# Kernel tuning notes

Measured on AMD Instinct MI355X. Metric: run time of the kernel, lower is better.

## Reference

```python
import jax, jax.numpy as jnp
import numpy as np

N_NODES, N_EDGES, N_ROOTS = 32768, 131072, 1024
VOCAB, EMB_D, FEAT = 50000, 256, 128
SEQ, HEADS, OUT_CH = 16, 16, 125
KERNELS = (5, 6, 7, 8)


def _add_self_loops(edge_index, n):
    loop = jnp.arange(n, dtype=edge_index.dtype)
    src = jnp.concatenate([edge_index[0], loop])
    dst = jnp.concatenate([edge_index[1], loop])
    return src, dst


def _gat_conv(x, W, a_src, a_dst, b, src, dst, n):
    # PyG GATConv (heads=1): h=xW, e_ij = LeakyReLU(a_s.h_j + a_d.h_i), softmax over incoming edges of i
    h = x @ W                                   # [N, F]
    al_s = h @ a_src                            # [N]
    al_d = h @ a_dst                            # [N]
    e = jax.nn.leaky_relu(al_s[src] + al_d[dst], 0.2)   # [E+N]
    m = jax.ops.segment_max(e, dst, num_segments=n)
    ex = jnp.exp(e - m[dst])
    den = jax.ops.segment_sum(ex, dst, num_segments=n)
    coef = ex / den[dst]
    out = jax.ops.segment_sum(coef[:, None] * h[src], dst, num_segments=n)
    return out + b


def _gcn_conv(x, W, b, src, dst, n):
    h = x @ W
    ones = jnp.ones_like(src, dtype=x.dtype)
    deg = jax.ops.segment_sum(ones, dst, num_segments=n)
    dinv = jax.lax.rsqrt(jnp.maximum(deg, 1.0))
    norm = dinv[src] * dinv[dst]                # [E+N]
    out = jax.ops.segment_sum(norm[:, None] * h[src], dst, num_segments=n)
    return out + b


def _transformer_block(x, Wq, bq, Wk, bk, Wv, bv, Wo, bo, g, be):
    # multi-head self-attention + output proj + residual + layernorm (attn_dropout=0)
    n, s, d = x.shape
    dh = d // HEADS
    q = (x @ Wq + bq).reshape(n, s, HEADS, dh)
    k = (x @ Wk + bk).reshape(n, s, HEADS, dh)
    v = (x @ Wv + bv).reshape(n, s, HEADS, dh)
    att = jnp.einsum('nqhd,nkhd->nhqk', q, k) / np.sqrt(dh).astype(np.float32)
    att = jax.nn.softmax(att, axis=-1)
    o = jnp.einsum('nhqk,nkhd->nqhd', att, v).reshape(n, s, d)
    o = o @ Wo + bo
    y = x + o
    mu = jnp.mean(y, axis=-1, keepdims=True)
    var = jnp.var(y, axis=-1, keepdims=True)
    return (y - mu) * jax.lax.rsqrt(var + 1e-5) * g + be


def _conv_branch(t, ws, bs):
    # t: [N, D, S]; Conv1d VALID + ReLU + max-pool over full output length
    feats = []
    for w, b in zip(ws, bs):
        a = jax.lax.conv_general_dilated(t, w, (1,), 'VALID',
                                         dimension_numbers=('NCH', 'OIH', 'NCH'))
        a = jax.nn.relu(a + b[:, None])
        feats.append(jnp.max(a, axis=-1))       # [N, OUT_CH]
    return jnp.concatenate(feats, axis=1)        # [N, 4*OUT_CH]


def _forward(x2, emb, Wq, bq, Wk, bk, Wv, bv, Wo, bo, ln_g, ln_b,
             gat1_W, gat1_as, gat1_ad, gat1_b, gcn1_W, gcn1_b,
             gat2_W, gat2_as, gat2_ad, gat2_b, gcn2_W, gcn2_b,
             conv_w0, conv_b0, conv_w1, conv_b1, conv_w2, conv_b2, conv_w3, conv_b3,
             fc1_W, fc1_b, fc2_W, fc2_b,
             text2, edge_index, root_index, rootpost_index):
    n = x2.shape[0]
    src, dst = _add_self_loops(edge_index, n)

    stance_graph = _gat_conv(x2, gat1_W, gat1_as, gat1_ad, gat1_b, src, dst, n)
    stance_shared = _gcn_conv(x2, gcn1_W, gcn1_b, src, dst, n)

    t = emb[text2]                                            # [N, S, D]
    t = _transformer_block(t, Wq, bq, Wk, bk, Wv, bv, Wo, bo, ln_g, ln_b)
    t_avg = jnp.mean(t, axis=1)                               # [N, D]

    cat = jnp.concatenate([stance_graph, stance_shared, t_avg], axis=1)  # [N, 2F+D]
    stance_graph2 = _gat_conv(cat, gat2_W, gat2_as, gat2_ad, gat2_b, src, dst, n)
    _ = _gcn_conv(stance_shared, gcn2_W, gcn2_b, src, dst, n)  # computed but unused in forward (faithful)

    tc = jnp.transpose(t, (0, 2, 1))                          # [N, D, S]
    text_feat = _conv_branch(tc, (conv_w0, conv_w1, conv_w2, conv_w3),
                             (conv_b0, conv_b1, conv_b2, conv_b3))  # [N, 500]

    final = jnp.concatenate([stance_graph2[root_index],
                             text_feat[root_index],
                             text_feat[rootpost_index]], axis=1)     # [B, F+1000]
    h = jax.nn.relu(final @ fc1_W + fc1_b)
    return h @ fc2_W + fc2_b                                  # [B, 3]


def setup_inputs() -> dict:
    key = jax.random.key(0)
    ks = iter(jax.random.split(key, 48))
    s = 0.05
    inp = {}
    inp['x2'] = jax.random.normal(next(ks), (N_NODES, FEAT), jnp.float32)
    inp['emb'] = jax.random.normal(next(ks), (VOCAB, EMB_D), jnp.float32) * s
    for nm in ['Wq', 'Wk', 'Wv', 'Wo']:
        inp[nm] = jax.random.normal(next(ks), (EMB_D, EMB_D), jnp.float32) * s
    for nm in ['bq', 'bk', 'bv', 'bo']:
        inp[nm] = jnp.zeros((EMB_D,), jnp.float32)
    inp['ln_g'] = jnp.ones((EMB_D,), jnp.float32)
    inp['ln_b'] = jnp.zeros((EMB_D,), jnp.float32)
    inp['gat1_W'] = jax.random.normal(next(ks), (FEAT, FEAT), jnp.float32) * s
    inp['gat1_as'] = jax.random.normal(next(ks), (FEAT,), jnp.float32) * s
    inp['gat1_ad'] = jax.random.normal(next(ks), (FEAT,), jnp.float32) * s
    inp['gat1_b'] = jnp.zeros((FEAT,), jnp.float32)
    inp['gcn1_W'] = jax.random.normal(next(ks), (FEAT, FEAT), jnp.float32) * s
    inp['gcn1_b'] = jnp.zeros((FEAT,), jnp.float32)
    inp['gat2_W'] = jax.random.normal(next(ks), (2 * FEAT + EMB_D, FEAT), jnp.float32) * s
    inp['gat2_as'] = jax.random.normal(next(ks), (FEAT,), jnp.float32) * s
    inp['gat2_ad'] = jax.random.normal(next(ks), (FEAT,), jnp.float32) * s
    inp['gat2_b'] = jnp.zeros((FEAT,), jnp.float32)
    inp['gcn2_W'] = jax.random.normal(next(ks), (FEAT, FEAT), jnp.float32) * s
    inp['gcn2_b'] = jnp.zeros((FEAT,), jnp.float32)
    for i, K in enumerate(KERNELS):
        inp[f'conv_w{i}'] = jax.random.normal(next(ks), (OUT_CH, EMB_D, K), jnp.float32) * s
        inp[f'conv_b{i}'] = jnp.zeros((OUT_CH,), jnp.float32)
    inp['fc1_W'] = jax.random.normal(next(ks), (FEAT + 8 * OUT_CH, 300), jnp.float32) * s
    inp['fc1_b'] = jnp.zeros((300,), jnp.float32)
    inp['fc2_W'] = jax.random.normal(next(ks), (300, 3), jnp.float32) * s
    inp['fc2_b'] = jnp.zeros((3,), jnp.float32)
    inp['text2'] = jax.random.randint(next(ks), (N_NODES, SEQ), 0, VOCAB, jnp.int32)
    inp['edge_index'] = jax.random.randint(next(ks), (2, N_EDGES), 0, N_NODES, jnp.int32)
    inp['root_index'] = jax.random.randint(next(ks), (N_ROOTS,), 0, N_NODES, jnp.int32)
    inp['rootpost_index'] = jax.random.randint(next(ks), (N_ROOTS,), 0, N_NODES, jnp.int32)
    return inp


def reference(x2, emb, Wq, bq, Wk, bk, Wv, bv, Wo, bo, ln_g, ln_b,
              gat1_W, gat1_as, gat1_ad, gat1_b, gcn1_W, gcn1_b,
              gat2_W, gat2_as, gat2_ad, gat2_b, gcn2_W, gcn2_b,
              conv_w0, conv_b0, conv_w1, conv_b1, conv_w2, conv_b2, conv_w3, conv_b3,
              fc1_W, fc1_b, fc2_W, fc2_b,
              text2, edge_index, root_index, rootpost_index):
    return _forward(x2, emb, Wq, bq, Wk, bk, Wv, bv, Wo, bo, ln_g, ln_b,
                    gat1_W, gat1_as, gat1_ad, gat1_b, gcn1_W, gcn1_b,
                    gat2_W, gat2_as, gat2_ad, gat2_b, gcn2_W, gcn2_b,
                    conv_w0, conv_b0, conv_w1, conv_b1, conv_w2, conv_b2, conv_w3, conv_b3,
                    fc1_W, fc1_b, fc2_W, fc2_b,
                    text2, edge_index, root_index, rootpost_index)
```

## Files before the change

### kernel.cpp

```cpp
#include <hip/hip_runtime.h>
#include <hip/hip_bf16.h>
#include <cstdint>
#include <cstddef>

#define N_NODES 32768
#define N_EDGES 131072
#define ET_EDGES (N_EDGES + N_NODES)
#define N_ROOTS 1024
#define EMB_D 256
#define FEAT 128
#define SEQ 16
#define OUT_CH 125

static inline int cdiv(long long a, long long b) { return (int)((a + b - 1) / b); }

typedef short short8 __attribute__((ext_vector_type(8)));
typedef short short4v __attribute__((ext_vector_type(4)));
typedef float f32x4 __attribute__((ext_vector_type(4)));

__device__ __forceinline__ float warpReduceSum(float v) {
#pragma unroll
    for (int m = 32; m; m >>= 1) v += __shfl_xor(v, m, 64);
    return v;
}
__device__ __forceinline__ int encf(float f) {
    int i = __float_as_int(f);
    return i >= 0 ? i : (i ^ 0x7fffffff);
}
__device__ __forceinline__ float decf(int i) {
    return __int_as_float(i >= 0 ? i : (i ^ 0x7fffffff));
}
__device__ __forceinline__ short f2bs(float x) {
    unsigned u = __float_as_uint(x);
    u += 0x7fffu + ((u >> 16) & 1u);
    return (short)(u >> 16);
}
__device__ __forceinline__ short2 f2bs2(float a, float b) {
    union {
        __hip_bfloat162 h;
        short2 s;
    } u;
    u.h = __float22bfloat162_rn(make_float2(a, b));
    return u.s;
}
__device__ __forceinline__ float bs2f(short s) {
    return __uint_as_float(((unsigned)(unsigned short)s) << 16);
}

__global__ void fill_i32(int* p, int v, int n) {
    int i = blockIdx.x * 256 + threadIdx.x;
    if (i < n) p[i] = v;
}

__global__ void init_cat(float* __restrict__ cat, const float* __restrict__ b1, const float* __restrict__ b2) {
    int i = blockIdx.x * 256 + threadIdx.x;
    int n = i >> 8, c = i & 255;
    float b = (c < 128) ? b1[c] : b2[c - 128];
    cat[(size_t)n * 512 + c] = b;
}

__global__ void repack_wall(const float* __restrict__ cw0, const float* __restrict__ cw1,
                            const float* __restrict__ cw2, const float* __restrict__ cw3,
                            __hip_bfloat16* __restrict__ wall) {
    int i = blockIdx.x * 256 + threadIdx.x;
    if (i >= 512 * 2048) return;
    int r = i >> 11, c = i & 2047;
    int k = c >> 8, ic = c & 255;
    float v = 0.f;
    if (r < 500) {
        int Kidx = r / 125, oc = r - Kidx * 125;
        int K = 5 + Kidx;
        if (k < K) {
            const float* cw = Kidx == 0 ? cw0 : Kidx == 1 ? cw1 : Kidx == 2 ? cw2 : cw3;
            v = cw[((size_t)oc * 256 + ic) * K + k];
        }
    }
    wall[i] = __float2bfloat16(v);
}

__global__ void repack_xf(const float* __restrict__ Wq, const float* __restrict__ Wk, const float* __restrict__ Wv,
                          const float* __restrict__ Wo, const float* __restrict__ bq, const float* __restrict__ bk,
                          const float* __restrict__ bv, short* __restrict__ wqkvT, short* __restrict__ woT,
                          float* __restrict__ bqkv) {
    int i = blockIdx.x * 256 + threadIdx.x;
    if (i < 768 * 256) {
        int n = i >> 8, k = i & 255;
        const float* W = n < 256 ? Wq : n < 512 ? Wk : Wv;
        wqkvT[i] = f2bs(W[k * 256 + (n & 255)]);
    }
    if (i < 256 * 256) {
        int n = i >> 8, k = i & 255;
        woT[i] = f2bs(Wo[k * 256 + n]);
    }
    if (i < 768) bqkv[i] = i < 256 ? bq[i] : i < 512 ? bk[i - 256] : bv[i - 512];
}

__global__ __launch_bounds__(256) void gemm64(const float* __restrict__ A, const float* __restrict__ B,
                                              const float* __restrict__ bias, float* __restrict__ C,
                                              int M, int N, int K, int lda, int ldc, int doRelu) {
    __shared__ float As[16][65];
    __shared__ float Bs[16][65];
    const int bm = blockIdx.y * 64, bn = blockIdx.x * 64;
    const int tid = threadIdx.x;
    const int tx = tid & 15, ty = tid >> 4;
    float acc[4][4] = {};
    for (int k0 = 0; k0 < K; k0 += 16) {
#pragma unroll
        for (int j = 0; j < 4; j++) {
            int i = tid + j * 256;
            int kk = i & 15, m = i >> 4;
            int gr = bm + m, gc = k0 + kk;
            As[kk][m] = (gr < M && gc < K) ? A[(size_t)gr * lda + gc] : 0.f;
        }
#pragma unroll
        for (int j = 0; j < 4; j++) {
            int i = tid + j * 256;
            int n = i & 63, kk = i >> 6;
            int gr = k0 + kk, gc = bn + n;
            Bs[kk][n] = (gr < K && gc < N) ? B[(size_t)gr * N + gc] : 0.f;
        }
        __syncthreads();
#pragma unroll
        for (int kk = 0; kk < 16; kk++) {
            float a[4], b[4];
#pragma unroll
            for (int i2 = 0; i2 < 4; i2++) a[i2] = As[kk][ty * 4 + i2];
#pragma unroll
            for (int j2 = 0; j2 < 4; j2++) b[j2] = Bs[kk][tx * 4 + j2];
#pragma unroll
            for (int i2 = 0; i2 < 4; i2++)
#pragma unroll
                for (int j2 = 0; j2 < 4; j2++) acc[i2][j2] = fmaf(a[i2], b[j2], acc[i2][j2]);
        }
        __syncthreads();
    }
#pragma unroll
    for (int i2 = 0; i2 < 4; i2++) {
        int r = bm + ty * 4 + i2;
        if (r >= M) continue;
#pragma unroll
        for (int j2 = 0; j2 < 4; j2++) {
            int c = bn + tx * 4 + j2;
            if (c >= N) continue;
            float v = acc[i2][j2];
            if (bias) v += bias[c];
            if (doRelu) v = fmaxf(v, 0.f);
            C[(size_t)r * ldc + c] = v;
        }
    }
}

__global__ __launch_bounds__(256) void alpha_kernel(const float* __restrict__ h, const float* __restrict__ asrc,
                                                    const float* __restrict__ adst, float* __restrict__ als,
                                                    float* __restrict__ ald) {
    int gw = (blockIdx.x * 256 + threadIdx.x) >> 6;
    int lane = threadIdx.x & 63;
    if (gw >= N_NODES) return;
    const float* row = h + (size_t)gw * FEAT;
    float v0 = row[lane], v1 = row[lane + 64];
    float ps = v0 * asrc[lane] + v1 * asrc[lane + 64];
    float pd = v0 * adst[lane] + v1 * adst[lane + 64];
    ps = warpReduceSum(ps);
    pd = warpReduceSum(pd);
    if (lane == 0) {
        als[gw] = ps;
        ald[gw] = pd;
    }
}

__device__ __forceinline__ void edge_decode(int i, const int* __restrict__ ei, int& s, int& d) {
    if (i < N_EDGES) {
        s = ei[i];
        d = ei[N_EDGES + i];
    } else {
        s = d = i - N_EDGES;
    }
}

__global__ void edge_p1(const int* __restrict__ ei, const float* __restrict__ als, const float* __restrict__ ald,
                        float* __restrict__ elog, int* __restrict__ menc, float* dega) {
    int i = blockIdx.x * 256 + threadIdx.x;
    if (i >= ET_EDGES) return;
    int s, d;
    edge_decode(i, ei, s, d);
    float e = als[s] + ald[d];
    e = (e >= 0.f) ? e : 0.2f * e;
    elog[i] = e;
    atomicMax(&menc[d], encf(e));
    if (dega) unsafeAtomicAdd(&dega[d], 1.f);
}

__global__ void edge_p2(const int* __restrict__ ei, float* __restrict__ elog, const int* __restrict__ menc,
                        float* __restrict__ den) {
    int i = blockIdx.x * 256 + threadIdx.x;
    if (i >= ET_EDGES) return;
    int s, d;
    edge_decode(i, ei, s, d);
    float ex = __expf(elog[i] - decf(menc[d]));
    elog[i] = ex;
    unsafeAtomicAdd(&den[d], ex);
}

__global__ void edge_p2b(const int* __restrict__ ei, float* __restrict__ elog, const float* __restrict__ den) {
    int i = blockIdx.x * 256 + threadIdx.x;
    if (i >= ET_EDGES) return;
    int s, d;
    edge_decode(i, ei, s, d);
    elog[i] = elog[i] / den[d];
}

__global__ void dinv_kernel(float* deg) {
    int i = blockIdx.x * 256 + threadIdx.x;
    if (i < N_NODES) deg[i] = rsqrtf(fmaxf(deg[i], 1.f));
}

__global__ void edge_scatter(const int* __restrict__ ei, const float* __restrict__ coef, const float* __restrict__ h,
                             float* __restrict__ out, int ldo) {
    int i = blockIdx.x * 256 + threadIdx.x;
    if (i >= ET_EDGES * FEAT) return;
    int e = i >> 7, f = i & 127;
    int s, d;
    edge_decode(e, ei, s, d);
    unsafeAtomicAdd(&out[(size_t)d * ldo + f], coef[e] * h[(size_t)s * FEAT + f]);
}

__global__ void gcn_scatter(const int* __restrict__ ei, const float* __restrict__ dinv, const float* __restrict__ h,
                            float* __restrict__ out, int ldo) {
    int i = blockIdx.x * 256 + threadIdx.x;
    if (i >= ET_EDGES * FEAT) return;
    int e = i >> 7, f = i & 127;
    int s, d;
    edge_decode(e, ei, s, d);
    float coef = dinv[s] * dinv[d];
    unsafeAtomicAdd(&out[(size_t)d * ldo + f], coef * h[(size_t)s * FEAT + f]);
}

__global__ void root_gather(const float* __restrict__ g2, const int* __restrict__ rooti, const float* __restrict__ gb,
                            float* __restrict__ fin) {
    int i = blockIdx.x * 256 + threadIdx.x;
    if (i >= N_ROOTS * FEAT) return;
    int r = i >> 7, c = i & 127;
    fin[(size_t)r * 1128 + c] = g2[(size_t)rooti[r] * FEAT + c] + gb[c];
}

__global__ void fc2_kernel(const float* __restrict__ fch, const float* __restrict__ W, const float* __restrict__ b,
                           float* __restrict__ out) {
    int i = blockIdx.x * 256 + threadIdx.x;
    if (i >= N_ROOTS * 3) return;
    int r = i / 3, c = i - r * 3;
    float acc = b[c];
    for (int k = 0; k < 300; k++) acc = fmaf(fch[(size_t)r * 300 + k], W[k * 3 + c], acc);
    out[i] = acc;
}

#define QA_STRIDE 264
#define KR_STRIDE 264

template <int MODE>
__global__ __launch_bounds__(256, 4) void xformer_kernel(
    const float* __restrict__ emb, const int* __restrict__ text2, const short* __restrict__ wqkvT,
    const float* __restrict__ bqkv, const short* __restrict__ woT, const float* __restrict__ bo,
    const float* __restrict__ lng, const float* __restrict__ lnb, const int* __restrict__ rooti,
    const int* __restrict__ rpi, float* __restrict__ cat, unsigned short* __restrict__ tbuf) {
    __shared__ short qa[32 * QA_STRIDE];
    __shared__ short kreg[32 * KR_STRIDE];

    const int tid = threadIdx.x;
    const int wave = tid >> 6, lane = tid & 63;
    const int quad = lane >> 4, l16 = lane & 15;

    int gnode[2];
#pragma unroll
    for (int m = 0; m < 2; m++) {
        int slot = blockIdx.x * 2 + m;
        gnode[m] = (MODE == 0) ? slot : ((slot < N_ROOTS) ? rooti[slot] : rpi[slot - N_ROOTS]);
    }
    const int tokA0 = text2[gnode[0] * SEQ + l16];
    const int tokA1 = text2[gnode[1] * SEQ + l16];

    short8 Areg[2][8];
#pragma unroll
    for (int k0 = 0; k0 < 8; k0++) {
        const float* pa0 = emb + (size_t)tokA0 * 256 + k0 * 32 + quad * 8;
        const float* pa1 = emb + (size_t)tokA1 * 256 + k0 * 32 + quad * 8;
        float4 a0l = ((const float4*)pa0)[0], a0h = ((const float4*)pa0)[1];
        float4 a1l = ((const float4*)pa1)[0], a1h = ((const float4*)pa1)[1];
        short2 c0 = f2bs2(a0l.x, a0l.y), c1 = f2bs2(a0l.z, a0l.w), c2 = f2bs2(a0h.x, a0h.y), c3 = f2bs2(a0h.z, a0h.w);
        Areg[0][k0] = (short8){c0.x, c0.y, c1.x, c1.y, c2.x, c2.y, c3.x, c3.y};
        c0 = f2bs2(a1l.x, a1l.y);
        c1 = f2bs2(a1l.z, a1l.w);
        c2 = f2bs2(a1h.x, a1h.y);
        c3 = f2bs2(a1h.z, a1h.w);
        Areg[1][k0] = (short8){c0.x, c0.y, c1.x, c1.y, c2.x, c2.y, c3.x, c3.y};
    }

    f32x4 vacc[4][2];

#pragma unroll
    for (int grp = 0; grp < 3; grp++) {
        f32x4 acc[4][2];
#pragma unroll
        for (int i = 0; i < 4; i++) {
            acc[i][0] = (f32x4){0.f, 0.f, 0.f, 0.f};
            acc[i][1] = (f32x4){0.f, 0.f, 0.f, 0.f};
        }
#pragma unroll
        for (int k0 = 0; k0 < 8; k0++) {
#pragma unroll
            for (int i = 0; i < 4; i++) {
                const int g = grp * 16 + wave * 4 + i;
                short8 B = *(const short8*)(wqkvT + (size_t)(g * 16 + l16) * 256 + k0 * 32 + quad * 8);
                acc[i][0] = __builtin_amdgcn_mfma_f32_16x16x32_bf16(Areg[0][k0], B, acc[i][0], 0, 0, 0);
                acc[i][1] = __builtin_amdgcn_mfma_f32_16x16x32_bf16(Areg[1][k0], B, acc[i][1], 0, 0, 0);
            }
        }
#pragma unroll
        for (int i = 0; i < 4; i++) {
            const int g = grp * 16 + wave * 4 + i;
            const int col = g * 16 + l16;
            const float b = bqkv[col];
            if (grp == 2) {
#pragma unroll
                for (int m = 0; m < 2; m++) {
                    vacc[i][m][0] = acc[i][m][0] + b;
                    vacc[i][m][1] = acc[i][m][1] + b;
                    vacc[i][m][2] = acc[i][m][2] + b;
                    vacc[i][m][3] = acc[i][m][3] + b;
                }
            } else {
#pragma unroll
                for (int m = 0; m < 2; m++) {
                    const int rbase = m * 16 + quad * 4;
                    float v0 = acc[i][m][0] + b, v1 = acc[i][m][1] + b;
                    float v2 = acc[i][m][2] + b, v3 = acc[i][m][3] + b;
                    if (grp == 0) {
                        v0 *= 0.25f;
                        v1 *= 0.25f;
                        v2 *= 0.25f;
                        v3 *= 0.25f;
                    }
                    short2 p01 = f2bs2(v0, v1), p23 = f2bs2(v2, v3);
                    short* dst = (grp == 0) ? (qa + (rbase)*QA_STRIDE + col) : (kreg + (rbase)*KR_STRIDE + (col - 256));
                    const int str = (grp == 0) ? QA_STRIDE : KR_STRIDE;
                    dst[0 * str] = p01.x;
                    dst[1 * str] = p01.y;
                    dst[2 * str] = p23.x;
                    dst[3 * str] = p23.y;
                }
            }
        }
    }

#pragma unroll
    for (int p = 0; p < 2; p++) {
#pragma unroll
        for (int i = 0; i < 4; i++) {
            const int h = wave * 4 + i;
            const int arow = p * 16 + l16;
            const int q8 = (quad & 1) * 8;
            short8 Af = *(const short8*)(kreg + arow * KR_STRIDE + h * 16 + q8);
            short8 Bf = *(const short8*)(qa + arow * QA_STRIDE + h * 16 + q8);
            if (quad >= 2) {
                Af = (short8){0, 0, 0, 0, 0, 0, 0, 0};
                Bf = (short8){0, 0, 0, 0, 0, 0, 0, 0};
            }
            f32x4 S = __builtin_amdgcn_mfma_f32_16x16x32_bf16(Af, Bf, (f32x4){0.f, 0.f, 0.f, 0.f}, 0, 0, 0);
            float mx = fmaxf(fmaxf(S[0], S[1]), fmaxf(S[2], S[3]));
            mx = fmaxf(mx, __shfl_xor(mx, 16));
            mx = fmaxf(mx, __shfl_xor(mx, 32));
            float e0 = __expf(S[0] - mx), e1 = __expf(S[1] - mx);
            float e2 = __expf(S[2] - mx), e3 = __expf(S[3] - mx);
            float sm = (e0 + e1) + (e2 + e3);
            sm += __shfl_xor(sm, 16);
            sm += __shfl_xor(sm, 32);
            const float inv = 1.f / sm;
            float pr[4] = {e0 * inv, e1 * inv, e2 * inv, e3 * inv};
            float bp[8];
#pragma unroll
            for (int j = 0; j < 8; j++) {
                const int srcq = (2 * quad + (j >> 2)) & 3;
                float v = __shfl(pr[j & 3], l16 + 16 * srcq);
                bp[j] = (quad < 2) ? v : 0.f;
            }
            short2 b01 = f2bs2(bp[0], bp[1]), b23 = f2bs2(bp[2], bp[3]);
            short2 b45 = f2bs2(bp[4], bp[5]), b67 = f2bs2(bp[6], bp[7]);
            short8 BP = (short8){b01.x, b01.y, b23.x, b23.y, b45.x, b45.y, b67.x, b67.y};
            float av[8];
#pragma unroll
            for (int j = 0; j < 8; j++) {
                const int srcq = ((quad & 1) * 2 + (j >> 2));
                float v = __shfl(vacc[i][p][j & 3], l16 + 16 * srcq);
                av[j] = (quad < 2) ? v : 0.f;
            }
            short2 a01 = f2bs2(av[0], av[1]), a23 = f2bs2(av[2], av[3]);
            short2 a45 = f2bs2(av[4], av[5]), a67 = f2bs2(av[6], av[7]);
            short8 Av = (short8){a01.x, a01.y, a23.x, a23.y, a45.x, a45.y, a67.x, a67.y};
            f32x4 O = __builtin_amdgcn_mfma_f32_16x16x32_bf16(Av, BP, (f32x4){0.f, 0.f, 0.f, 0.f}, 0, 0, 0);
            short2 o01 = f2bs2(O[0], O[1]), o23 = f2bs2(O[2], O[3]);
            *(short4v*)(qa + arow * QA_STRIDE + h * 16 + quad * 4) = (short4v){o01.x, o01.y, o23.x, o23.y};
        }
    }
    __syncthreads();

    {
        short8 Afr[2][8];
#pragma unroll
        for (int m = 0; m < 2; m++)
#pragma unroll
            for (int k0 = 0; k0 < 8; k0++)
                Afr[m][k0] = *(const short8*)(qa + (m * 16 + l16) * QA_STRIDE + k0 * 32 + quad * 8);
#pragma unroll
        for (int i = 0; i < 4; i++) {
            const int g = wave * 4 + i;
            f32x4 oa0 = (f32x4){0.f, 0.f, 0.f, 0.f}, oa1 = (f32x4){0.f, 0.f, 0.f, 0.f};
#pragma unroll
            for (int k0 = 0; k0 < 8; k0++) {
                short8 B = *(const short8*)(woT + (size_t)(g * 16 + l16) * 256 + k0 * 32 + quad * 8);
                oa0 = __builtin_amdgcn_mfma_f32_16x16x32_bf16(Afr[0][k0], B, oa0, 0, 0, 0);
                oa1 = __builtin_amdgcn_mfma_f32_16x16x32_bf16(Afr[1][k0], B, oa1, 0, 0, 0);
            }
            const int col = g * 16 + l16;
            const float bocol = bo[col];
            short2 a01 = f2bs2(oa0[0] + bocol, oa0[1] + bocol), a23 = f2bs2(oa0[2] + bocol, oa0[3] + bocol);
            short2 c01 = f2bs2(oa1[0] + bocol, oa1[1] + bocol), c23 = f2bs2(oa1[2] + bocol, oa1[3] + bocol);
            kreg[(quad * 4 + 0) * KR_STRIDE + col] = a01.x;
            kreg[(quad * 4 + 1) * KR_STRIDE + col] = a01.y;
            kreg[(quad * 4 + 2) * KR_STRIDE + col] = a23.x;
            kreg[(quad * 4 + 3) * KR_STRIDE + col] = a23.y;
            kreg[(16 + quad * 4 + 0) * KR_STRIDE + col] = c01.x;
            kreg[(16 + quad * 4 + 1) * KR_STRIDE + col] = c01.y;
            kreg[(16 + quad * 4 + 2) * KR_STRIDE + col] = c23.x;
            kreg[(16 + quad * 4 + 3) * KR_STRIDE + col] = c23.y;
        }
    }
    __syncthreads();

    float* qs = (float*)qa;
    {
        const int row = tid >> 3, seg = tid & 7;
        const int m = row >> 4, r = row & 15;
        const int tokr = text2[gnode[m] * SEQ + r];
        const float* ep = emb + (size_t)tokr * 256 + seg * 32;
        float sum = 0.f, sq = 0.f;
#pragma unroll
        for (int j = 0; j < 4; j++) {
            short8 y8 = *(const short8*)(kreg + row * KR_STRIDE + seg * 32 + j * 8);
            float4 ea = ((const float4*)(ep + j * 8))[0];
            float4 eb = ((const float4*)(ep + j * 8))[1];
            float ev[8] = {ea.x, ea.y, ea.z, ea.w, eb.x, eb.y, eb.z, eb.w};
            float yv[8];
#pragma unroll
            for (int e = 0; e < 8; e++) {
                yv[e] = bs2f(y8[e]) + ev[e];
                sum += yv[e];
                sq = fmaf(yv[e], yv[e], sq);
            }
            short2 w0 = f2bs2(yv[0], yv[1]), w1 = f2bs2(yv[2], yv[3]);
            short2 w2 = f2bs2(yv[4], yv[5]), w3 = f2bs2(yv[6], yv[7]);
            *(short4v*)(kreg + row * KR_STRIDE + seg * 32 + j * 8) = (short4v){w0.x, w0.y, w1.x, w1.y};
            *(short4v*)(kreg + row * KR_STRIDE + seg * 32 + j * 8 + 4) = (short4v){w2.x, w2.y, w3.x, w3.y};
        }
        qs[tid] = sum;
        qs[256 + tid] = sq;
    }
    __syncthreads();
    if (tid < 32) {
        float s = 0.f, q2 = 0.f;
#pragma unroll
        for (int j = 0; j < 8; j++) {
            s += qs[tid * 8 + j];
            q2 += qs[256 + tid * 8 + j];
        }
        float mu = s * (1.f / 256.f);
        float var = q2 * (1.f / 256.f) - mu * mu;
        qs[512 + tid * 2] = mu;
        qs[512 + tid * 2 + 1] = rsqrtf(var + 1e-5f);
    }
    __syncthreads();
    {
        const int c = tid;
        const float g = lng[c], bb = lnb[c];
        float csum[2] = {0.f, 0.f};
#pragma unroll
        for (int m = 0; m < 2; m++) {
#pragma unroll
            for (int r = 0; r < 16; r++) {
                const int row = m * 16 + r;
                const float yv = bs2f(kreg[row * KR_STRIDE + c]);
                const float mu = qs[512 + row * 2], rstd = qs[512 + row * 2 + 1];
                const float o = (yv - mu) * rstd * g + bb;
                if (MODE == 0) {
                    csum[m] += o;
                } else {
                    tbuf[((size_t)(blockIdx.x * 2 + m) * 24 + r) * 256 + c] = (unsigned short)f2bs(o);
                }
            }
        }
        if (MODE == 0) {
            cat[(size_t)gnode[0] * 512 + 256 + c] = csum[0] * (1.f / 16.f);
            cat[(size_t)gnode[1] * 512 + 256 + c] = csum[1] * (1.f / 16.f);
        } else {
            for (int z = tid; z < 2 * 8 * 256; z += 256) {
                const int m = z >> 11, rem = z & 2047;
                tbuf[((size_t)(blockIdx.x * 2 + m) * 24 + 16 + (rem >> 8)) * 256 + (rem & 255)] = 0;
            }
        }
    }
}

__global__ __launch_bounds__(256) void conv_gemm(const short* __restrict__ tb, const short* __restrict__ wall,
                                                 float* __restrict__ C) {
    __shared__ short As[128 * 40];
    __shared__ short Bs[128 * 40];
    const int bid = blockIdx.x;
    const int m0 = (bid >> 2) * 128;
    const int n0 = (bid & 3) * 128;
    const int tid = threadIdx.x;
    const int lane = tid & 63;
    const int wave = tid >> 6;
    const int wm = (wave >> 1) * 64, wn = (wave & 1) * 64;
    const int quad = lane >> 4, l16 = lane & 15;

    const int r0 = tid >> 2, kc = (tid & 3) * 8;
    const int r1 = r0 + 64;
    const int am0 = m0 + r0, am1 = m0 + r1;
    const int s0 = am0 / 12, p0_ = am0 - s0 * 12;
    const int s1 = am1 / 12, p1_ = am1 - s1 * 12;
    const size_t ga0 = (size_t)(s0 * 24 + p0_) * 256 + kc;
    const size_t ga1 = (size_t)(s1 * 24 + p1_) * 256 + kc;
    const size_t gb0 = (size_t)(n0 + r0) * 2048 + kc;
    const size_t gb1 = (size_t)(n0 + r1) * 2048 + kc;
    short* sa0 = As + r0 * 40 + kc;
    short* sa1 = As + r1 * 40 + kc;
    short* sb0 = Bs + r0 * 40 + kc;
    short* sb1 = Bs + r1 * 40 + kc;

    f32x4 acc[4][4];
#pragma unroll
    for (int i = 0; i < 4; i++)
#pragma unroll
        for (int j = 0; j < 4; j++) acc[i][j] = (f32x4){0.f, 0.f, 0.f, 0.f};

    for (int k0 = 0; k0 < 2048; k0 += 32) {
        short8 a0 = *(const short8*)(tb + ga0 + k0);
        short8 a1 = *(const short8*)(tb + ga1 + k0);
        short8 b0 = *(const short8*)(wall + gb0 + k0);
        short8 b1 = *(const short8*)(wall + gb1 + k0);
        *(short8*)sa0 = a0;
        *(short8*)sa1 = a1;
        *(short8*)sb0 = b0;
        *(short8*)sb1 = b1;
        __syncthreads();
        short8 af[4], bfr[4];
#pragma unroll
        for (int i = 0; i < 4; i++) af[i] = *(const short8*)(As + (wm + i * 16 + l16) * 40 + quad * 8);
#pragma unroll
        for (int j = 0; j < 4; j++) bfr[j] = *(const short8*)(Bs + (wn + j * 16 + l16) * 40 + quad * 8);
#pragma unroll
        for (int i = 0; i < 4; i++)
#pragma unroll
            for (int j = 0; j < 4; j++)
                acc[i][j] = __builtin_amdgcn_mfma_f32_16x16x32_bf16(af[i], bfr[j], acc[i][j], 0, 0, 0);
        __syncthreads();
    }
#pragma unroll
    for (int i = 0; i < 4; i++) {
#pragma unroll
        for (int j = 0; j < 4; j++) {
            const int col = n0 + wn + j * 16 + l16;
            const size_t base = (size_t)(m0 + wm + i * 16 + quad * 4) * 512 + col;
#pragma unroll
            for (int r = 0; r < 4; r++) C[base + (size_t)r * 512] = acc[i][j][r];
        }
    }
}

__global__ void conv_maxpool(const float* __restrict__ C, const float* __restrict__ cb0, const float* __restrict__ cb1,
                             const float* __restrict__ cb2, const float* __restrict__ cb3, float* __restrict__ fin) {
    int i = blockIdx.x * 256 + threadIdx.x;
    if (i >= 2048 * 500) return;
    int slot = i / 500, q = i - slot * 500;
    int Kidx = q / 125, oc = q - Kidx * 125;
    int L = 12 - Kidx;
    const float* base = C + (size_t)(slot * 12) * 512 + q;
    float m = base[0];
    for (int p = 1; p < L; p++) m = fmaxf(m, base[(size_t)p * 512]);
    float b = (Kidx == 0 ? cb0 : Kidx == 1 ? cb1 : Kidx == 2 ? cb2 : cb3)[oc];
    float v = fmaxf(m + b, 0.f);
    int idx = slot < N_ROOTS ? slot : slot - N_ROOTS;
    int colbase = slot < N_ROOTS ? 128 : 628;
    fin[(size_t)idx * 1128 + colbase + q] = v;
}

extern "C" void kernel_launch(void* const* d_in, const int* in_sizes, int n_in, void* d_out, int out_size, void* d_ws,
                              size_t ws_size, hipStream_t stream) {
    const float* x2 = (const float*)d_in[0];
    const float* emb = (const float*)d_in[1];
    const float* Wq = (const float*)d_in[2];
    const float* Wk = (const float*)d_in[3];
    const float* Wv = (const float*)d_in[4];
    const float* Wo = (const float*)d_in[5];
    const float* bq = (const float*)d_in[6];
    const float* bk = (const float*)d_in[7];
    const float* bv = (const float*)d_in[8];
    const float* bo = (const float*)d_in[9];
    const float* lng = (const float*)d_in[10];
    const float* lnb = (const float*)d_in[11];
    const float* gat1_W = (const float*)d_in[12];
    const float* gat1_as = (const float*)d_in[13];
    const float* gat1_ad = (const float*)d_in[14];
    const float* gat1_b = (const float*)d_in[15];
    const float* gcn1_W = (const float*)d_in[16];
    const float* gcn1_b = (const float*)d_in[17];
    const float* gat2_W = (const float*)d_in[18];
    const float* gat2_as = (const float*)d_in[19];
    const float* gat2_ad = (const float*)d_in[20];
    const float* gat2_b = (const float*)d_in[21];
    const float* cw0 = (const float*)d_in[24];
    const float* cb0 = (const float*)d_in[25];
    const float* cw1 = (const float*)d_in[26];
    const float* cb1 = (const float*)d_in[27];
    const float* cw2 = (const float*)d_in[28];
    const float* cb2 = (const float*)d_in[29];
    const float* cw3 = (const float*)d_in[30];
    const float* cb3 = (const float*)d_in[31];
    const float* fc1_W = (const float*)d_in[32];
    const float* fc1_b = (const float*)d_in[33];
    const float* fc2_W = (const float*)d_in[34];
    const float* fc2_b = (const float*)d_in[35];
    const int* text2 = (const int*)d_in[36];
    const int* ei = (const int*)d_in[37];
    const int* rooti = (const int*)d_in[38];
    const int* rpi = (const int*)d_in[39];

    float* ws = (float*)d_ws;
    size_t off = 0;
    auto alloc = [&](size_t n) {
        float* p = ws + off;
        off += n;
        return p;
    };
    float* g2o = alloc((size_t)N_NODES * FEAT);
    float* den1 = alloc(N_NODES);
    float* den2 = alloc(N_NODES);
    float* deg = alloc(N_NODES);
    size_t zero_floats = off;
    float* cat = alloc((size_t)N_NODES * 512);
    float* h1 = alloc((size_t)N_NODES * FEAT);
    float* h2 = alloc((size_t)N_NODES * FEAT);
    float* hg2 = alloc((size_t)N_NODES * FEAT);
    float* als1 = alloc(N_NODES);
    float* ald1 = alloc(N_NODES);
    float* als2 = alloc(N_NODES);
    float* ald2 = alloc(N_NODES);
    int* m1 = (int*)alloc(N_NODES);
    int* m2 = (int*)alloc(N_NODES);
    float* el1 = alloc(ET_EDGES);
    float* el2 = alloc(ET_EDGES);
    float* fin = alloc((size_t)N_ROOTS * 1128);
    float* fch = alloc((size_t)N_ROOTS * 300);
    float* wallf = alloc(512 * 2048 / 2);
    float* wqkvTf = alloc(768 * 256 / 2);
    float* woTf = alloc(256 * 256 / 2);
    float* bqkv = alloc(768);
    (void)ws_size;
    (void)in_sizes;
    (void)n_in;
    (void)out_size;

    unsigned short* tbuf = (unsigned short*)h1;
    __hip_bfloat16* wall = (__hip_bfloat16*)wallf;
    short* wqkvT = (short*)wqkvTf;
    short* woT = (short*)woTf;
    float* Cbuf = cat;

    hipMemsetAsync(g2o, 0, zero_floats * sizeof(float), stream);
    init_cat<<<cdiv((long long)N_NODES * 256, 256), 256, 0, stream>>>(cat, gat1_b, gcn1_b);
    fill_i32<<<cdiv(2 * N_NODES, 256), 256, 0, stream>>>(m1, (int)0x80000000, 2 * N_NODES);
    repack_wall<<<cdiv(512 * 2048, 256), 256, 0, stream>>>(cw0, cw1, cw2, cw3, wall);
    repack_xf<<<cdiv(768 * 256, 256), 256, 0, stream>>>(Wq, Wk, Wv, Wo, bq, bk, bv, wqkvT, woT, bqkv);

    gemm64<<<dim3(2, 512), 256, 0, stream>>>(x2, gat1_W, nullptr, h1, N_NODES, FEAT, FEAT, FEAT, FEAT, 0);
    gemm64<<<dim3(2, 512), 256, 0, stream>>>(x2, gcn1_W, nullptr, h2, N_NODES, FEAT, FEAT, FEAT, FEAT, 0);
    alpha_kernel<<<cdiv((long long)N_NODES * 64, 256), 256, 0, stream>>>(h1, gat1_as, gat1_ad, als1, ald1);
    edge_p1<<<cdiv(ET_EDGES, 256), 256, 0, stream>>>(ei, als1, ald1, el1, m1, deg);
    edge_p2<<<cdiv(ET_EDGES, 256), 256, 0, stream>>>(ei, el1, m1, den1);
    edge_p2b<<<cdiv(ET_EDGES, 256), 256, 0, stream>>>(ei, el1, den1);
    dinv_kernel<<<cdiv(N_NODES, 256), 256, 0, stream>>>(deg);
    const int sc_blocks = cdiv((long long)ET_EDGES * FEAT, 256);
    edge_scatter<<<sc_blocks, 256, 0, stream>>>(ei, el1, h1, cat + 0, 512);
    gcn_scatter<<<sc_blocks, 256, 0, stream>>>(ei, deg, h2, cat + 128, 512);
    xformer_kernel<0><<<N_NODES / 2, 256, 0, stream>>>(emb, text2, wqkvT, bqkv, woT, bo, lng, lnb, rooti, rpi, cat,
                                                       nullptr);
    xformer_kernel<1><<<2 * N_ROOTS / 2, 256, 0, stream>>>(emb, text2, wqkvT, bqkv, woT, bo, lng, lnb, rooti, rpi,
                                                           nullptr, tbuf);
    gemm64<<<dim3(2, 512), 256, 0, stream>>>(cat, gat2_W, nullptr, hg2, N_NODES, FEAT, 512, 512, FEAT, 0);
    alpha_kernel<<<cdiv((long long)N_NODES * 64, 256), 256, 0, stream>>>(hg2, gat2_as, gat2_ad, als2, ald2);
    edge_p1<<<cdiv(ET_EDGES, 256), 256, 0, stream>>>(ei, als2, ald2, el2, m2, nullptr);
    edge_p2<<<cdiv(ET_EDGES, 256), 256, 0, stream>>>(ei, el2, m2, den2);
    edge_p2b<<<cdiv(ET_EDGES, 256), 256, 0, stream>>>(ei, el2, den2);
    edge_scatter<<<sc_blocks, 256, 0, stream>>>(ei, el2, hg2, g2o, FEAT);
    conv_gemm<<<192 * 4, 256, 0, stream>>>((const short*)tbuf, (const short*)wall, Cbuf);
    root_gather<<<cdiv(N_ROOTS * FEAT, 256), 256, 0, stream>>>(g2o, rooti, gat2_b, fin);
    conv_maxpool<<<cdiv(2048 * 500, 256), 256, 0, stream>>>(Cbuf, cb0, cb1, cb2, cb3, fin);
    gemm64<<<dim3(cdiv(300, 64), cdiv(N_ROOTS, 64)), 256, 0, stream>>>(fin, fc1_W, fc1_b, fch, N_ROOTS, 300, 1128,
                                                                       1128, 300, 1);
    fc2_kernel<<<cdiv(N_ROOTS * 3, 256), 256, 0, stream>>>(fch, fc2_W, fc2_b, (float*)d_out);
}
```

Measured before the change: 2.327 ms.

## Use bf16 MFMA GEMM for graph linears and stage attention operands through LDS

```diff
diff --git a/kernel.cpp b/kernel.cpp
--- a/kernel.cpp
+++ b/kernel.cpp
@@ -93,6 +93,69 @@
         woT[i] = f2bs(Wo[k * 256 + n]);
     }
     if (i < 768) bqkv[i] = i < 256 ? bq[i] : i < 512 ? bk[i - 256] : bv[i - 512];
+}
+
+__global__ void repack_wT(const float* __restrict__ W, short* __restrict__ out, int K, int N) {
+    int i = blockIdx.x * 256 + threadIdx.x;
+    if (i >= K * N) return;
+    int n = i / K, k = i - n * K;
+    out[i] = f2bs(W[(size_t)k * N + n]);
+}
+
+__global__ __launch_bounds__(256) void mfma_gemm_n128(const float* __restrict__ A, const short* __restrict__ Wt,
+                                                      float* __restrict__ C, int K) {
+    __shared__ short As[128 * 40];
+    __shared__ short Bs[128 * 40];
+    const int m0 = blockIdx.x * 128;
+    const int tid = threadIdx.x;
+    const int lane = tid & 63;
+    const int wave = tid >> 6;
+    const int wm = (wave >> 1) * 64, wn = (wave & 1) * 64;
+    const int quad = lane >> 4, l16 = lane & 15;
+
+    const int r0 = tid >> 2, kc = (tid & 3) * 8;
+    const int r1 = r0 + 64;
+
+    f32x4 acc[4][4];
+#pragma unroll
+    for (int i = 0; i < 4; i++)
+#pragma unroll
+        for (int j = 0; j < 4; j++) acc[i][j] = (f32x4){0.f, 0.f, 0.f, 0.f};
+
+    for (int k0 = 0; k0 < K; k0 += 32) {
+#pragma unroll
+        for (int rr = 0; rr < 2; rr++) {
+            const int r = rr ? r1 : r0;
+            const float* pa = A + (size_t)(m0 + r) * K + k0 + kc;
+            float4 a0 = ((const float4*)pa)[0], a1 = ((const float4*)pa)[1];
+            short2 c0 = f2bs2(a0.x, a0.y), c1 = f2bs2(a0.z, a0.w), c2 = f2bs2(a1.x, a1.y), c3 = f2bs2(a1.z, a1.w);
+            *(short8*)(As + r * 40 + kc) = (short8){c0.x, c0.y, c1.x, c1.y, c2.x, c2.y, c3.x, c3.y};
+        }
+        *(short8*)(Bs + r0 * 40 + kc) = *(const short8*)(Wt + (size_t)r0 * K + k0 + kc);
+        *(short8*)(Bs + r1 * 40 + kc) = *(const short8*)(Wt + (size_t)r1 * K + k0 + kc);
+        __syncthreads();
+        short8 af[4], bfr[4];
+#pragma unroll
+        for (int i = 0; i < 4; i++) af[i] = *(const short8*)(As + (wm + i * 16 + l16) * 40 + quad * 8);
+#pragma unroll
+        for (int j = 0; j < 4; j++) bfr[j] = *(const short8*)(Bs + (wn + j * 16 + l16) * 40 + quad * 8);
+#pragma unroll
+        for (int i = 0; i < 4; i++)
+#pragma unroll
+            for (int j = 0; j < 4; j++)
+                acc[i][j] = __builtin_amdgcn_mfma_f32_16x16x32_bf16(af[i], bfr[j], acc[i][j], 0, 0, 0);
+        __syncthreads();
+    }
+#pragma unroll
+    for (int i = 0; i < 4; i++) {
+#pragma unroll
+        for (int j = 0; j < 4; j++) {
+            const int col = wn + j * 16 + l16;
+            const size_t base = (size_t)(m0 + wm + i * 16 + quad * 4) * 128 + col;
+#pragma unroll
+            for (int r = 0; r < 4; r++) C[base + (size_t)r * 128] = acc[i][j][r];
+        }
+    }
 }
 
 __global__ __launch_bounds__(256) void gemm64(const float* __restrict__ A, const float* __restrict__ B,
@@ -256,6 +319,10 @@
 #define QA_STRIDE 264
 #define KR_STRIDE 264
 
+__device__ __forceinline__ int vt_addr(int d, int key) {
+    return d * 32 + (((key & 24) ^ (((d ^ (d >> 2)) & 3) << 3)) | (key & 7));
+}
+
 template <int MODE>
 __global__ __launch_bounds__(256, 4) void xformer_kernel(
     const float* __restrict__ emb, const int* __restrict__ text2, const short* __restrict__ wqkvT,
@@ -340,7 +407,7 @@
                         v3 *= 0.25f;
                     }
                     short2 p01 = f2bs2(v0, v1), p23 = f2bs2(v2, v3);
-                    short* dst = (grp == 0) ? (qa + (rbase)*QA_STRIDE + col) : (kreg + (rbase)*KR_STRIDE + (col - 256));
+                    short* dst = (grp == 0) ? (qa + rbase * QA_STRIDE + col) : (kreg + rbase * KR_STRIDE + (col - 256));
                     const int str = (grp == 0) ? QA_STRIDE : KR_STRIDE;
                     dst[0 * str] = p01.x;
                     dst[1 * str] = p01.y;
@@ -374,27 +441,36 @@
             sm += __shfl_xor(sm, 16);
             sm += __shfl_xor(sm, 32);
             const float inv = 1.f / sm;
-            float pr[4] = {e0 * inv, e1 * inv, e2 * inv, e3 * inv};
-            float bp[8];
-#pragma unroll
-            for (int j = 0; j < 8; j++) {
-                const int srcq = (2 * quad + (j >> 2)) & 3;
-                float v = __shfl(pr[j & 3], l16 + 16 * srcq);
-                bp[j] = (quad < 2) ? v : 0.f;
+            short2 p01 = f2bs2(e0 * inv, e1 * inv), p23 = f2bs2(e2 * inv, e3 * inv);
+            *(short4v*)(qa + arow * QA_STRIDE + h * 16 + quad * 4) = (short4v){p01.x, p01.y, p23.x, p23.y};
+        }
+    }
+    __syncthreads();
+
+#pragma unroll
+    for (int i = 0; i < 4; i++) {
+        const int d = (wave * 4 + i) * 16 + l16;
+#pragma unroll
+        for (int m = 0; m < 2; m++) {
+            const int rbase = m * 16 + quad * 4;
+            short2 p01 = f2bs2(vacc[i][m][0], vacc[i][m][1]), p23 = f2bs2(vacc[i][m][2], vacc[i][m][3]);
+            *(short4v*)(kreg + vt_addr(d, rbase)) = (short4v){p01.x, p01.y, p23.x, p23.y};
+        }
+    }
+
+#pragma unroll
+    for (int p = 0; p < 2; p++) {
+#pragma unroll
+        for (int i = 0; i < 4; i++) {
+            const int h = wave * 4 + i;
+            const int arow = p * 16 + l16;
+            const int q8 = (quad & 1) * 8;
+            short8 BP = *(const short8*)(qa + arow * QA_STRIDE + h * 16 + q8);
+            short8 Av = *(const short8*)(kreg + vt_addr(h * 16 + l16, p * 16 + q8));
+            if (quad >= 2) {
+                BP = (short8){0, 0, 0, 0, 0, 0, 0, 0};
+                Av = (short8){0, 0, 0, 0, 0, 0, 0, 0};
             }
-            short2 b01 = f2bs2(bp[0], bp[1]), b23 = f2bs2(bp[2], bp[3]);
-            short2 b45 = f2bs2(bp[4], bp[5]), b67 = f2bs2(bp[6], bp[7]);
-            short8 BP = (short8){b01.x, b01.y, b23.x, b23.y, b45.x, b45.y, b67.x, b67.y};
-            float av[8];
-#pragma unroll
-            for (int j = 0; j < 8; j++) {
-                const int srcq = ((quad & 1) * 2 + (j >> 2));
-                float v = __shfl(vacc[i][p][j & 3], l16 + 16 * srcq);
-                av[j] = (quad < 2) ? v : 0.f;
-            }
-            short2 a01 = f2bs2(av[0], av[1]), a23 = f2bs2(av[2], av[3]);
-            short2 a45 = f2bs2(av[4], av[5]), a67 = f2bs2(av[6], av[7]);
-            short8 Av = (short8){a01.x, a01.y, a23.x, a23.y, a45.x, a45.y, a67.x, a67.y};
             f32x4 O = __builtin_amdgcn_mfma_f32_16x16x32_bf16(Av, BP, (f32x4){0.f, 0.f, 0.f, 0.f}, 0, 0, 0);
             short2 o01 = f2bs2(O[0], O[1]), o23 = f2bs2(O[2], O[3]);
             *(short4v*)(qa + arow * QA_STRIDE + h * 16 + quad * 4) = (short4v){o01.x, o01.y, o23.x, o23.y};
@@ -663,6 +739,9 @@
     float* wqkvTf = alloc(768 * 256 / 2);
     float* woTf = alloc(256 * 256 / 2);
     float* bqkv = alloc(768);
+    float* wg1Tf = alloc(128 * 128 / 2);
+    float* wc1Tf = alloc(128 * 128 / 2);
+    float* wg2Tf = alloc(128 * 512 / 2);
     (void)ws_size;
     (void)in_sizes;
     (void)n_in;
@@ -672,6 +751,9 @@
     __hip_bfloat16* wall = (__hip_bfloat16*)wallf;
     short* wqkvT = (short*)wqkvTf;
     short* woT = (short*)woTf;
+    short* wg1T = (short*)wg1Tf;
+    short* wc1T = (short*)wc1Tf;
+    short* wg2T = (short*)wg2Tf;
     float* Cbuf = cat;
 
     hipMemsetAsync(g2o, 0, zero_floats * sizeof(float), stream);
@@ -679,9 +761,12 @@
     fill_i32<<<cdiv(2 * N_NODES, 256), 256, 0, stream>>>(m1, (int)0x80000000, 2 * N_NODES);
     repack_wall<<<cdiv(512 * 2048, 256), 256, 0, stream>>>(cw0, cw1, cw2, cw3, wall);
     repack_xf<<<cdiv(768 * 256, 256), 256, 0, stream>>>(Wq, Wk, Wv, Wo, bq, bk, bv, wqkvT, woT, bqkv);
-
-    gemm64<<<dim3(2, 512), 256, 0, stream>>>(x2, gat1_W, nullptr, h1, N_NODES, FEAT, FEAT, FEAT, FEAT, 0);
-    gemm64<<<dim3(2, 512), 256, 0, stream>>>(x2, gcn1_W, nullptr, h2, N_NODES, FEAT, FEAT, FEAT, FEAT, 0);
+    repack_wT<<<cdiv(128 * 128, 256), 256, 0, stream>>>(gat1_W, wg1T, 128, 128);
+    repack_wT<<<cdiv(128 * 128, 256), 256, 0, stream>>>(gcn1_W, wc1T, 128, 128);
+    repack_wT<<<cdiv(512 * 128, 256), 256, 0, stream>>>(gat2_W, wg2T, 512, 128);
+
+    mfma_gemm_n128<<<N_NODES / 128, 256, 0, stream>>>(x2, wg1T, h1, 128);
+    mfma_gemm_n128<<<N_NODES / 128, 256, 0, stream>>>(x2, wc1T, h2, 128);
     alpha_kernel<<<cdiv((long long)N_NODES * 64, 256), 256, 0, stream>>>(h1, gat1_as, gat1_ad, als1, ald1);
     edge_p1<<<cdiv(ET_EDGES, 256), 256, 0, stream>>>(ei, als1, ald1, el1, m1, deg);
     edge_p2<<<cdiv(ET_EDGES, 256), 256, 0, stream>>>(ei, el1, m1, den1);
@@ -694,7 +779,7 @@
                                                        nullptr);
     xformer_kernel<1><<<2 * N_ROOTS / 2, 256, 0, stream>>>(emb, text2, wqkvT, bqkv, woT, bo, lng, lnb, rooti, rpi,
                                                            nullptr, tbuf);
-    gemm64<<<dim3(2, 512), 256, 0, stream>>>(cat, gat2_W, nullptr, hg2, N_NODES, FEAT, 512, 512, FEAT, 0);
+    mfma_gemm_n128<<<N_NODES / 128, 256, 0, stream>>>(cat, wg2T, hg2, 512);
     alpha_kernel<<<cdiv((long long)N_NODES * 64, 256), 256, 0, stream>>>(hg2, gat2_as, gat2_ad, als2, ald2);
     edge_p1<<<cdiv(ET_EDGES, 256), 256, 0, stream>>>(ei, als2, ald2, el2, m2, nullptr);
     edge_p2<<<cdiv(ET_EDGES, 256), 256, 0, stream>>>(ei, el2, m2, den2);
```

Measured after the change: 2.184 ms. -6.2%, faster.
